# Kernel tuning notes

Hardware: AMD Instinct MI355X
Metric: run time of the kernel (lower is better)

## Reference

```python
import jax, jax.numpy as jnp
import numpy as np

N_NODES = 10000
N_EDGES = 320000
N_PAIRS = 8192
IN_CH = 128
HIDDEN = 256
OUT_CH = 1


def setup_inputs() -> dict:
    key = jax.random.key(0)
    k1, k2, k3, k4, k5 = jax.random.split(key, 5)
    x = jax.random.normal(k1, (N_NODES, IN_CH), dtype=jnp.float32)
    edge_index = jax.random.randint(k2, (2, N_EDGES), 0, N_NODES, dtype=jnp.int64)
    tar_ei = jax.random.randint(k3, (2, N_PAIRS), 0, N_NODES, dtype=jnp.int64)
    # xsmlp params (Linear(2*in, hidden) -> ReLU -> Linear(hidden, out))
    W1 = jax.random.normal(k4, (HIDDEN, 2 * IN_CH), dtype=jnp.float32) * (1.0 / np.sqrt(2 * IN_CH))
    b1 = jnp.zeros((HIDDEN,), dtype=jnp.float32)
    W2 = jax.random.normal(k5, (OUT_CH, HIDDEN), dtype=jnp.float32) * (1.0 / np.sqrt(HIDDEN))
    b2 = jnp.zeros((OUT_CH,), dtype=jnp.float32)
    return {"x": x, "edge_index": edge_index, "tar_ei": tar_ei,
            "W1": W1, "b1": b1, "W2": W2, "b2": b2}


def reference(x, edge_index, tar_ei, W1, b1, W2, b2):
    # k=2 path of NCNPredictor.
    N = x.shape[0]
    # Symmetric binary adjacency (coalesce + fill_value_(1.0) => values all 1).
    A = (jnp.zeros((N, N), dtype=x.dtype)
         .at[edge_index[0], edge_index[1]].set(1.0)
         .at[edge_index[1], edge_index[0]].set(1.0))
    i, j = tar_ei[0], tar_ei[1]
    # xij: elementwise product of endpoint features  [B, d]
    xij = x[i] * x[j]
    # Common-neighbor indicator rows: cn_1_1 = adj1[tar_i] * adj1[tar_j]  [B, N]
    cn = A[i] * A[j]
    # spmm_add(cn_1_1, x): sum features of common neighbors  [B, d]
    cn_emb = cn @ x
    xs = jnp.concatenate([xij, cn_emb], axis=-1)  # [B, 2d]
    # xs.relu() in the original is not in-place -> no-op, faithfully omitted.
    h = jax.nn.relu(xs @ W1.T + b1)
    return h @ W2.T + b2
```

## Files before the change

### kernel.cpp

```cpp
#include <hip/hip_runtime.h>

#define N_NODES 10000
#define N_EDGES 320000
#define N_PAIRS 8192
#define IN_CH   128
#define HIDDEN  256
#define K_DIM   256
#define WPR     320
#define WPR4    (WPR / 4)
#define TILE_B  16
#define CN_CAP  128
#define ZERO_BLOCKS (N_NODES * WPR / 4 / 256)
#define PACK_BLOCKS 32
#define ADJ_BLOCKS  (N_EDGES / 256)

typedef __attribute__((ext_vector_type(8))) short  short8;
typedef __attribute__((ext_vector_type(4))) float  f32x4;

static __device__ inline short f2bf(float f) {
    union { float f; unsigned u; } c; c.f = f;
    unsigned r = (c.u + 0x7FFFu + ((c.u >> 16) & 1u)) >> 16;
    return (short)r;
}

__global__ __launch_bounds__(256) void zero_pack_kernel(uint4* __restrict__ adj4,
                                                        const float* __restrict__ W1,
                                                        short* __restrict__ W1B) {
    int bid = blockIdx.x;
    int tid = threadIdx.x;
    if (bid < ZERO_BLOCKS) {
        adj4[(size_t)bid * 256 + tid] = make_uint4(0u, 0u, 0u, 0u);
    } else {
        int t2 = (bid - ZERO_BLOCKS) * 256 + tid;
        int ks = t2 >> 10;
        int t  = (t2 >> 6) & 15;
        int l  = t2 & 63;
        int n  = t * 16 + (l & 15);
        int kb = ks * 32 + ((l >> 4) << 3);
        const float* src = W1 + (size_t)n * K_DIM + kb;
        short* dst = W1B + ((size_t)(ks * 16 + t) * 64 + l) * 8;
#pragma unroll
        for (int e = 0; e < 8; ++e) dst[e] = f2bf(src[e]);
    }
}

__global__ __launch_bounds__(256) void build_adj_kernel(const int* __restrict__ ei,
                                                        unsigned int* __restrict__ adj) {
    int e = blockIdx.x * blockDim.x + threadIdx.x;
    int u = ei[e];
    int v = ei[N_EDGES + e];
    atomicOr(&adj[(size_t)u * WPR + (v >> 5)], 1u << (v & 31));
    atomicOr(&adj[(size_t)v * WPR + (u >> 5)], 1u << (u & 31));
}

__global__ __launch_bounds__(512) void fused_kernel(const float* __restrict__ x,
                                                    const int* __restrict__ tei,
                                                    const unsigned int* __restrict__ adj,
                                                    const short* __restrict__ W1B,
                                                    const float* __restrict__ b1,
                                                    const float* __restrict__ W2,
                                                    const float* __restrict__ b2,
                                                    float* __restrict__ out) {
    __shared__ float4 s_xs4[TILE_B * 64];
    __shared__ int    s_ij[TILE_B][2];
    __shared__ int    s_cnt[TILE_B];
    __shared__ int    s_cnl[TILE_B][CN_CAP];
    __shared__ float  s_part[TILE_B][8];

    const int tid = threadIdx.x;
    const int p0 = blockIdx.x * TILE_B;

    if (tid < TILE_B) {
        s_ij[tid][0] = tei[p0 + tid];
        s_ij[tid][1] = tei[N_PAIRS + p0 + tid];
        s_cnt[tid] = 0;
    }
    {
        int zb = tid >> 5, zu = 32 + (tid & 31);
        s_xs4[zb * 64 + zu] = make_float4(0.f, 0.f, 0.f, 0.f);
    }
    __syncthreads();

    const int b = tid >> 5;
    const int s = tid & 31;
    const int i = s_ij[b][0];
    const int j = s_ij[b][1];

    const float4* xi4 = (const float4*)(x + (size_t)i * IN_CH);
    const float4* xj4 = (const float4*)(x + (size_t)j * IN_CH);
    float4 va = xi4[s];
    float4 vb = xj4[s];

    const uint4* ri4 = (const uint4*)(adj + (size_t)i * WPR);
    const uint4* rj4 = (const uint4*)(adj + (size_t)j * WPR);
    for (int q = s; q < WPR4; q += 32) {
        uint4 a = ri4[q];
        uint4 c = rj4[q];
        unsigned int m[4] = { a.x & c.x, a.y & c.y, a.z & c.z, a.w & c.w };
#pragma unroll
        for (int ww = 0; ww < 4; ++ww) {
            unsigned int mm = m[ww];
            while (mm) {
                int bit = __builtin_ctz(mm);
                mm &= mm - 1;
                int n = q * 128 + ww * 32 + bit;
                int pos = atomicAdd(&s_cnt[b], 1);
                if (pos < CN_CAP) {
                    s_cnl[b][pos] = n;
                } else {
                    const float* xn = x + (size_t)n * IN_CH;
                    for (int d = 0; d < IN_CH; ++d) {
                        int u = 32 + (d >> 2);
                        float* base = (float*)&s_xs4[b * 64 + (u ^ (b & 7))];
                        atomicAdd(&base[d & 3], xn[d]);
                    }
                }
            }
        }
    }

    s_xs4[b * 64 + (s ^ (b & 7))] =
        make_float4(va.x * vb.x, va.y * vb.y, va.z * vb.z, va.w * vb.w);

    {
        int cnt = s_cnt[b];
        if (cnt > CN_CAP) cnt = CN_CAP;
        int u = (32 + s) ^ (b & 7);
        float4 d0 = s_xs4[b * 64 + u];
        float4 d1 = make_float4(0.f, 0.f, 0.f, 0.f);
        float4 d2 = make_float4(0.f, 0.f, 0.f, 0.f);
        float4 d3 = make_float4(0.f, 0.f, 0.f, 0.f);
        int c = 0;
        for (; c + 4 <= cnt; c += 4) {
            const float4* q0 = (const float4*)(x + (size_t)s_cnl[b][c]     * IN_CH);
            const float4* q1 = (const float4*)(x + (size_t)s_cnl[b][c + 1] * IN_CH);
            const float4* q2 = (const float4*)(x + (size_t)s_cnl[b][c + 2] * IN_CH);
            const float4* q3 = (const float4*)(x + (size_t)s_cnl[b][c + 3] * IN_CH);
            float4 v0 = q0[s], v1 = q1[s], v2 = q2[s], v3 = q3[s];
            d0 = make_float4(d0.x + v0.x, d0.y + v0.y, d0.z + v0.z, d0.w + v0.w);
            d1 = make_float4(d1.x + v1.x, d1.y + v1.y, d1.z + v1.z, d1.w + v1.w);
            d2 = make_float4(d2.x + v2.x, d2.y + v2.y, d2.z + v2.z, d2.w + v2.w);
            d3 = make_float4(d3.x + v3.x, d3.y + v3.y, d3.z + v3.z, d3.w + v3.w);
        }
        for (; c < cnt; ++c) {
            const float4* q0 = (const float4*)(x + (size_t)s_cnl[b][c] * IN_CH);
            float4 v0 = q0[s];
            d0 = make_float4(d0.x + v0.x, d0.y + v0.y, d0.z + v0.z, d0.w + v0.w);
        }
        d0 = make_float4(d0.x + d1.x + d2.x + d3.x,
                         d0.y + d1.y + d2.y + d3.y,
                         d0.z + d1.z + d2.z + d3.z,
                         d0.w + d1.w + d2.w + d3.w);
        s_xs4[b * 64 + u] = d0;
    }
    __syncthreads();

    const int w    = tid >> 6;
    const int lane = tid & 63;
    const int t0 = w * 2;
    const int mr = lane & 15;
    const int kb = lane >> 4;

    f32x4 acc0 = {0.f, 0.f, 0.f, 0.f};
    f32x4 acc1 = {0.f, 0.f, 0.f, 0.f};

    const short8* W1B8 = (const short8*)W1B;
#pragma unroll
    for (int ks = 0; ks < 8; ++ks) {
        int f0 = ks * 8 + kb * 2;
        float4 x0 = s_xs4[mr * 64 + (f0 ^ (mr & 7))];
        float4 x1 = s_xs4[mr * 64 + ((f0 + 1) ^ (mr & 7))];
        short8 af;
        af[0] = f2bf(x0.x); af[1] = f2bf(x0.y); af[2] = f2bf(x0.z); af[3] = f2bf(x0.w);
        af[4] = f2bf(x1.x); af[5] = f2bf(x1.y); af[6] = f2bf(x1.z); af[7] = f2bf(x1.w);
        int fb = (ks * 16 + t0) * 64 + lane;
        short8 bf0 = W1B8[fb];
        short8 bf1 = W1B8[fb + 64];
        acc0 = __builtin_amdgcn_mfma_f32_16x16x32_bf16(af, bf0, acc0, 0, 0, 0);
        acc1 = __builtin_amdgcn_mfma_f32_16x16x32_bf16(af, bf1, acc1, 0, 0, 0);
    }

    const int ncol = lane & 15;
    const float b10 = b1[t0 * 16 + ncol];
    const float b11 = b1[(t0 + 1) * 16 + ncol];
    const float w20 = W2[t0 * 16 + ncol];
    const float w21 = W2[(t0 + 1) * 16 + ncol];

    float sum[4];
#pragma unroll
    for (int r = 0; r < 4; ++r)
        sum[r] = w20 * fmaxf(acc0[r] + b10, 0.f) + w21 * fmaxf(acc1[r] + b11, 0.f);

#pragma unroll
    for (int r = 0; r < 4; ++r) {
        float v = sum[r];
        v += __shfl_xor(v, 1);
        v += __shfl_xor(v, 2);
        v += __shfl_xor(v, 4);
        v += __shfl_xor(v, 8);
        if ((lane & 15) == 0) s_part[kb * 4 + r][w] = v;
    }
    __syncthreads();

    if (tid < TILE_B) {
        float r = b2[0];
#pragma unroll
        for (int ww = 0; ww < 8; ++ww) r += s_part[tid][ww];
        out[p0 + tid] = r;
    }
}

extern "C" void kernel_launch(void* const* d_in, const int* in_sizes, int n_in,
                              void* d_out, int out_size, void* d_ws, size_t ws_size,
                              hipStream_t stream) {
    const float* x   = (const float*)d_in[0];
    const int*   ei  = (const int*)d_in[1];
    const int*   tei = (const int*)d_in[2];
    const float* W1  = (const float*)d_in[3];
    const float* b1  = (const float*)d_in[4];
    const float* W2  = (const float*)d_in[5];
    const float* b2  = (const float*)d_in[6];
    float* out = (float*)d_out;

    unsigned char* ws = (unsigned char*)d_ws;
    const size_t adj_bytes = (size_t)N_NODES * WPR * sizeof(unsigned int);
    unsigned int* adj = (unsigned int*)ws;
    short* W1B = (short*)(ws + adj_bytes);

    zero_pack_kernel<<<ZERO_BLOCKS + PACK_BLOCKS, 256, 0, stream>>>((uint4*)adj, W1, W1B);
    build_adj_kernel<<<ADJ_BLOCKS, 256, 0, stream>>>(ei, adj);
    fused_kernel<<<N_PAIRS / TILE_B, 512, 0, stream>>>(x, tei, adj, W1B, b1, W2, b2, out);
}
```

Measured before the change: 54.06 us.

## Overlap xij half of first GEMM with adjacency build in a mixed kernel

Splits the first-layer GEMM into two K halves. The xij half is computed in a new mixed kernel that also runs the edge atomicOr adjacency build in separate blocks, so the two independent jobs overlap. Partial accumulators go to a workspace buffer and are reloaded by the second kernel, which only does the common-neighbour half. The cost is extra global traffic for the partial sums, plus a larger grid of heterogeneous blocks in the middle kernel.

```diff
diff --git a/kernel.cpp b/kernel.cpp
--- a/kernel.cpp
+++ b/kernel.cpp
@@ -12,7 +12,8 @@
 #define CN_CAP  128
 #define ZERO_BLOCKS (N_NODES * WPR / 4 / 256)
 #define PACK_BLOCKS 32
-#define ADJ_BLOCKS  (N_EDGES / 256)
+#define XIJ_BLOCKS  (N_PAIRS / TILE_B)
+#define BUILD_BLOCKS (N_EDGES / 512)
 
 typedef __attribute__((ext_vector_type(8))) short  short8;
 typedef __attribute__((ext_vector_type(4))) float  f32x4;
@@ -44,24 +45,72 @@
     }
 }
 
-__global__ __launch_bounds__(256) void build_adj_kernel(const int* __restrict__ ei,
-                                                        unsigned int* __restrict__ adj) {
-    int e = blockIdx.x * blockDim.x + threadIdx.x;
-    int u = ei[e];
-    int v = ei[N_EDGES + e];
-    atomicOr(&adj[(size_t)u * WPR + (v >> 5)], 1u << (v & 31));
-    atomicOr(&adj[(size_t)v * WPR + (u >> 5)], 1u << (u & 31));
-}
-
-__global__ __launch_bounds__(512) void fused_kernel(const float* __restrict__ x,
+__global__ __launch_bounds__(512) void mixed_kernel(const float* __restrict__ x,
                                                     const int* __restrict__ tei,
-                                                    const unsigned int* __restrict__ adj,
+                                                    const int* __restrict__ ei,
+                                                    unsigned int* __restrict__ adj,
                                                     const short* __restrict__ W1B,
-                                                    const float* __restrict__ b1,
-                                                    const float* __restrict__ W2,
-                                                    const float* __restrict__ b2,
-                                                    float* __restrict__ out) {
-    __shared__ float4 s_xs4[TILE_B * 64];
+                                                    f32x4* __restrict__ K1) {
+    const int tid = threadIdx.x;
+    if (blockIdx.x >= XIJ_BLOCKS) {
+        int e = (blockIdx.x - XIJ_BLOCKS) * 512 + tid;
+        int u = ei[e];
+        int v = ei[N_EDGES + e];
+        atomicOr(&adj[(size_t)u * WPR + (v >> 5)], 1u << (v & 31));
+        atomicOr(&adj[(size_t)v * WPR + (u >> 5)], 1u << (u & 31));
+        return;
+    }
+
+    __shared__ float4 s_xij[TILE_B * 32];
+    const int p0 = blockIdx.x * TILE_B;
+
+    const int b = tid >> 5;
+    const int s = tid & 31;
+    const int i = tei[p0 + b];
+    const int j = tei[N_PAIRS + p0 + b];
+    float4 va = ((const float4*)(x + (size_t)i * IN_CH))[s];
+    float4 vb = ((const float4*)(x + (size_t)j * IN_CH))[s];
+    s_xij[b * 32 + (s ^ (b & 7))] =
+        make_float4(va.x * vb.x, va.y * vb.y, va.z * vb.z, va.w * vb.w);
+    __syncthreads();
+
+    const int w    = tid >> 6;
+    const int lane = tid & 63;
+    const int t0 = w * 2;
+    const int mr = lane & 15;
+    const int kb = lane >> 4;
+
+    f32x4 acc0 = {0.f, 0.f, 0.f, 0.f};
+    f32x4 acc1 = {0.f, 0.f, 0.f, 0.f};
+    const short8* W1B8 = (const short8*)W1B;
+#pragma unroll
+    for (int ks = 0; ks < 4; ++ks) {
+        int f0 = ks * 8 + kb * 2;
+        float4 x0 = s_xij[mr * 32 + (f0 ^ (mr & 7))];
+        float4 x1 = s_xij[mr * 32 + ((f0 + 1) ^ (mr & 7))];
+        short8 af;
+        af[0] = f2bf(x0.x); af[1] = f2bf(x0.y); af[2] = f2bf(x0.z); af[3] = f2bf(x0.w);
+        af[4] = f2bf(x1.x); af[5] = f2bf(x1.y); af[6] = f2bf(x1.z); af[7] = f2bf(x1.w);
+        int fb = (ks * 16 + t0) * 64 + lane;
+        short8 bf0 = W1B8[fb];
+        short8 bf1 = W1B8[fb + 64];
+        acc0 = __builtin_amdgcn_mfma_f32_16x16x32_bf16(af, bf0, acc0, 0, 0, 0);
+        acc1 = __builtin_amdgcn_mfma_f32_16x16x32_bf16(af, bf1, acc1, 0, 0, 0);
+    }
+    K1[((blockIdx.x * 8 + w) * 2 + 0) * 64 + lane] = acc0;
+    K1[((blockIdx.x * 8 + w) * 2 + 1) * 64 + lane] = acc1;
+}
+
+__global__ __launch_bounds__(512) void fused2_kernel(const float* __restrict__ x,
+                                                     const int* __restrict__ tei,
+                                                     const unsigned int* __restrict__ adj,
+                                                     const short* __restrict__ W1B,
+                                                     const f32x4* __restrict__ K1,
+                                                     const float* __restrict__ b1,
+                                                     const float* __restrict__ W2,
+                                                     const float* __restrict__ b2,
+                                                     float* __restrict__ out) {
+    __shared__ float4 s_cn[TILE_B * 32];
     __shared__ int    s_ij[TILE_B][2];
     __shared__ int    s_cnt[TILE_B];
     __shared__ int    s_cnl[TILE_B][CN_CAP];
@@ -76,8 +125,8 @@
         s_cnt[tid] = 0;
     }
     {
-        int zb = tid >> 5, zu = 32 + (tid & 31);
-        s_xs4[zb * 64 + zu] = make_float4(0.f, 0.f, 0.f, 0.f);
+        int zb = tid >> 5, zu = tid & 31;
+        s_cn[zb * 32 + zu] = make_float4(0.f, 0.f, 0.f, 0.f);
     }
     __syncthreads();
 
@@ -85,11 +134,6 @@
     const int s = tid & 31;
     const int i = s_ij[b][0];
     const int j = s_ij[b][1];
-
-    const float4* xi4 = (const float4*)(x + (size_t)i * IN_CH);
-    const float4* xj4 = (const float4*)(x + (size_t)j * IN_CH);
-    float4 va = xi4[s];
-    float4 vb = xj4[s];
 
     const uint4* ri4 = (const uint4*)(adj + (size_t)i * WPR);
     const uint4* rj4 = (const uint4*)(adj + (size_t)j * WPR);
@@ -110,8 +154,8 @@
                 } else {
                     const float* xn = x + (size_t)n * IN_CH;
                     for (int d = 0; d < IN_CH; ++d) {
-                        int u = 32 + (d >> 2);
-                        float* base = (float*)&s_xs4[b * 64 + (u ^ (b & 7))];
+                        int u = d >> 2;
+                        float* base = (float*)&s_cn[b * 32 + (u ^ (b & 7))];
                         atomicAdd(&base[d & 3], xn[d]);
                     }
                 }
@@ -119,14 +163,11 @@
         }
     }
 
-    s_xs4[b * 64 + (s ^ (b & 7))] =
-        make_float4(va.x * vb.x, va.y * vb.y, va.z * vb.z, va.w * vb.w);
-
     {
         int cnt = s_cnt[b];
         if (cnt > CN_CAP) cnt = CN_CAP;
-        int u = (32 + s) ^ (b & 7);
-        float4 d0 = s_xs4[b * 64 + u];
+        int u = s ^ (b & 7);
+        float4 d0 = s_cn[b * 32 + u];
         float4 d1 = make_float4(0.f, 0.f, 0.f, 0.f);
         float4 d2 = make_float4(0.f, 0.f, 0.f, 0.f);
         float4 d3 = make_float4(0.f, 0.f, 0.f, 0.f);
@@ -151,7 +192,7 @@
                          d0.y + d1.y + d2.y + d3.y,
                          d0.z + d1.z + d2.z + d3.z,
                          d0.w + d1.w + d2.w + d3.w);
-        s_xs4[b * 64 + u] = d0;
+        s_cn[b * 32 + u] = d0;
     }
     __syncthreads();
 
@@ -161,15 +202,15 @@
     const int mr = lane & 15;
     const int kb = lane >> 4;
 
-    f32x4 acc0 = {0.f, 0.f, 0.f, 0.f};
-    f32x4 acc1 = {0.f, 0.f, 0.f, 0.f};
+    f32x4 acc0 = K1[((blockIdx.x * 8 + w) * 2 + 0) * 64 + lane];
+    f32x4 acc1 = K1[((blockIdx.x * 8 + w) * 2 + 1) * 64 + lane];
 
     const short8* W1B8 = (const short8*)W1B;
 #pragma unroll
-    for (int ks = 0; ks < 8; ++ks) {
-        int f0 = ks * 8 + kb * 2;
-        float4 x0 = s_xs4[mr * 64 + (f0 ^ (mr & 7))];
-        float4 x1 = s_xs4[mr * 64 + ((f0 + 1) ^ (mr & 7))];
+    for (int ks = 4; ks < 8; ++ks) {
+        int f0 = ks * 8 + kb * 2 - 32;
+        float4 x0 = s_cn[mr * 32 + (f0 ^ (mr & 7))];
+        float4 x1 = s_cn[mr * 32 + ((f0 + 1) ^ (mr & 7))];
         short8 af;
         af[0] = f2bf(x0.x); af[1] = f2bf(x0.y); af[2] = f2bf(x0.z); af[3] = f2bf(x0.w);
         af[4] = f2bf(x1.x); af[5] = f2bf(x1.y); af[6] = f2bf(x1.z); af[7] = f2bf(x1.w);
@@ -226,8 +267,9 @@
     const size_t adj_bytes = (size_t)N_NODES * WPR * sizeof(unsigned int);
     unsigned int* adj = (unsigned int*)ws;
     short* W1B = (short*)(ws + adj_bytes);
+    f32x4* K1  = (f32x4*)(ws + adj_bytes + 256 * 1024);
 
     zero_pack_kernel<<<ZERO_BLOCKS + PACK_BLOCKS, 256, 0, stream>>>((uint4*)adj, W1, W1B);
-    build_adj_kernel<<<ADJ_BLOCKS, 256, 0, stream>>>(ei, adj);
-    fused_kernel<<<N_PAIRS / TILE_B, 512, 0, stream>>>(x, tei, adj, W1B, b1, W2, b2, out);
-}
+    mixed_kernel<<<XIJ_BLOCKS + BUILD_BLOCKS, 512, 0, stream>>>(x, tei, ei, adj, W1B, K1);
+    fused2_kernel<<<XIJ_BLOCKS, 512, 0, stream>>>(x, tei, adj, W1B, K1, b1, W2, b2, out);
+}
```

Result: slower. 56.31 us (+4.2%).
